# Kernel optimization log

Measured on AMD Instinct MI355X. Metric: run time of the kernel, lower is better.

## Reference

```python
import jax, jax.numpy as jnp
import numpy as np

B, S, T = 32, 512, 512
SRC_SIZE, TGT_SIZE, OUT_SIZE, NUM_HEAD = 2048, 1024, 1024, 8
HEAD_DIM = OUT_SIZE // NUM_HEAD  # 128


def setup_inputs() -> dict:
    key = jax.random.key(0)
    ks = jax.random.split(key, 12)
    src = jax.random.normal(ks[0], (B, S, SRC_SIZE), dtype=jnp.float32)
    tgt = jax.random.normal(ks[1], (B, T, TGT_SIZE), dtype=jnp.float32)
    # binary float masks (1=valid, 0=pad); guarantee at least one valid src per row
    src_mask = (jax.random.uniform(ks[2], (B, S)) > 0.3).astype(jnp.float32)
    src_mask = src_mask.at[:, 0].set(1.0)
    tgt_mask = (jax.random.uniform(ks[3], (B, T)) > 0.3).astype(jnp.float32)
    tgt_mask = tgt_mask.at[:, 0].set(1.0)
    # FCNet in this repo is weight_norm(Linear) with no activation at drop=0 -> plain Linear
    def lin(k, out_f, in_f):
        return jax.random.normal(k, (out_f, in_f), dtype=jnp.float32) / np.sqrt(in_f)
    W_src = lin(ks[4], 2 * OUT_SIZE, SRC_SIZE)
    b_src = jnp.zeros((2 * OUT_SIZE,), jnp.float32)
    W_tgt = lin(ks[5], OUT_SIZE, TGT_SIZE)
    b_tgt = jnp.zeros((OUT_SIZE,), jnp.float32)
    W_out = lin(ks[6], OUT_SIZE, OUT_SIZE + TGT_SIZE)
    b_out = jnp.zeros((OUT_SIZE,), jnp.float32)
    return {"src": src, "tgt": tgt, "src_mask": src_mask, "tgt_mask": tgt_mask,
            "W_src": W_src, "b_src": b_src, "W_tgt": W_tgt, "b_tgt": b_tgt,
            "W_out": W_out, "b_out": b_out}


def reference(src, tgt, src_mask, tgt_mask, W_src, b_src, W_tgt, b_tgt, W_out, b_out):
    b, s, _ = src.shape
    t = tgt.shape[1]
    # projections (FCNet == Linear here)
    src_trans = jnp.einsum('bsf,of->bso', src, W_src) + b_src        # [B,S,2D]
    tgt_trans = jnp.einsum('btf,of->bto', tgt, W_tgt) + b_tgt        # [B,T,D]
    src_trans = src_trans * src_mask[:, :, None]
    tgt_trans = tgt_trans * tgt_mask[:, :, None]
    src_key, src_val = jnp.split(src_trans, 2, axis=2)               # each [B,S,D]
    # contiguous per-head chunks == reshape
    k = src_key.reshape(b, s, NUM_HEAD, HEAD_DIM)
    v = src_val.reshape(b, s, NUM_HEAD, HEAD_DIM)
    q = tgt_trans.reshape(b, t, NUM_HEAD, HEAD_DIM)
    scores = jnp.einsum('bthd,bshd->bhts', q, k) / np.sqrt(HEAD_DIM)  # [B,H,T,S]
    scores = jnp.where(src_mask[:, None, None, :] == 0, -jnp.inf, scores)
    attn = jax.nn.softmax(scores, axis=-1)
    tgt_update = jnp.einsum('bhts,bshd->bthd', attn, v).reshape(b, t, OUT_SIZE)
    cat_tgt = jnp.concatenate([tgt, tgt_update], axis=2)             # [B,T,TGT+D]
    return jnp.einsum('btf,of->bto', cat_tgt, W_out) + b_out         # [B,T,D]
```

## Files before the change

kernel.cpp:

```cpp
#include <hip/hip_runtime.h>

typedef __attribute__((ext_vector_type(4))) float f32x4;
typedef __attribute__((ext_vector_type(8))) short short8;
typedef unsigned short u16;

__device__ __forceinline__ u16 f2bf(float f) {
  unsigned int u = __float_as_uint(f);
  return (u16)((u + 0x7fffu + ((u >> 16) & 1u)) >> 16);
}

__device__ __forceinline__ void gload16(const void* g, void* l) {
  __builtin_amdgcn_global_load_lds((const __attribute__((address_space(1))) void*)g,
                                   (__attribute__((address_space(3))) void*)l, 16, 0, 0);
}

__global__ void cvt_f32_bf16(const float* __restrict__ in, u16* __restrict__ out, int n4) {
  int i = blockIdx.x * blockDim.x + threadIdx.x;
  int stride = gridDim.x * blockDim.x;
  for (; i < n4; i += stride) {
    float4 v = ((const float4*)in)[i];
    ushort4 o;
    o.x = f2bf(v.x); o.y = f2bf(v.y); o.z = f2bf(v.z); o.w = f2bf(v.w);
    ((ushort4*)out)[i] = o;
  }
}

__global__ void cvt_tgt_strided(const float* __restrict__ in, u16* __restrict__ cat, int n4) {
  int i = blockIdx.x * blockDim.x + threadIdx.x;
  int stride = gridDim.x * blockDim.x;
  for (; i < n4; i += stride) {
    int e = i * 4;
    int row = e >> 10;
    int c = e & 1023;
    float4 v = ((const float4*)in)[i];
    ushort4 o;
    o.x = f2bf(v.x); o.y = f2bf(v.y); o.z = f2bf(v.z); o.w = f2bf(v.w);
    *(ushort4*)(cat + (size_t)row * 2048 + c) = o;
  }
}

template <bool MASK, bool OUTBF, bool VSPLIT>
__global__ __launch_bounds__(512) void gemm256(const u16* __restrict__ A, int lda,
                                               const u16* __restrict__ W,
                                               const float* __restrict__ bias,
                                               const float* __restrict__ rowmask,
                                               void* __restrict__ Cout, int ldc,
                                               int nbn, int K,
                                               u16* __restrict__ vTout) {
  __shared__ __align__(16) u16 lds[2 * 32768];
  const int tid = threadIdx.x;
  const int lane = tid & 63;
  const int wid = tid >> 6;
  const int lr = lane & 15, lh = lane >> 4;
  const int wm = wid >> 2;
  const int wn = wid & 3;

  const int nwg = gridDim.x;
  const int cpx = nwg >> 3;
  const int bid = (blockIdx.x & 7) * cpx + (blockIdx.x >> 3);
  const int bm = bid / nbn;
  const int bn = bid - bm * nbn;

  const int srow = tid >> 3;
  const int scol = ((tid & 7) ^ (srow & 7)) << 3;
  const u16* As0 = A + (size_t)(bm * 256 + srow) * lda + scol;
  const u16* Ws0 = W + (size_t)(bn * 256 + srow) * K + scol;

  auto stageA = [&](int h, int t, int buf) {
    char* d = (char*)lds + buf * 65536 + h * 16384 + tid * 16;
    const u16* s = As0 + (size_t)(h * 128) * lda + t * 64;
    gload16(s, d);
    gload16(s + (size_t)64 * lda, d + 8192);
  };
  auto stageB = [&](int h, int t, int buf) {
    char* d = (char*)lds + buf * 65536 + 32768 + h * 16384 + tid * 16;
    const u16* s = Ws0 + (size_t)(h * 128) * K + t * 64;
    gload16(s, d);
    gload16(s + (size_t)64 * K, d + 8192);
  };

  const int key = (lr & 7) << 4;
  const int sb0 = ((0 + lh) << 4) ^ key;
  const int sb1 = ((4 + lh) << 4) ^ key;
  const int arow = (wm * 64 + lr) * 128;
  const int brow = 32768 + (wn * 32 + lr) * 128;

  f32x4 acc[8][4];
#pragma unroll
  for (int m = 0; m < 8; ++m)
#pragma unroll
    for (int n = 0; n < 4; ++n) acc[m][n] = (f32x4){0.f, 0.f, 0.f, 0.f};

  const int NT = K >> 6;

  stageA(0, 0, 0); stageB(0, 0, 0); stageB(1, 0, 0); stageA(1, 0, 0);
  asm volatile("s_waitcnt vmcnt(4)" ::: "memory");
  __builtin_amdgcn_s_barrier();
  __builtin_amdgcn_sched_barrier(0);

  for (int t = 0; t < NT; ++t) {
    const int cur = t & 1, nxt = cur ^ 1;
    const char* Lb = (const char*)lds + cur * 65536;
    const bool pf = (t + 1 < NT);

    short8 a[4][2], b0[2][2], b1[2][2];

#pragma unroll
    for (int m = 0; m < 4; ++m) {
      a[m][0] = *(const short8*)(Lb + arow + m * 2048 + sb0);
      a[m][1] = *(const short8*)(Lb + arow + m * 2048 + sb1);
    }
#pragma unroll
    for (int n = 0; n < 2; ++n) {
      b0[n][0] = *(const short8*)(Lb + brow + n * 2048 + sb0);
      b0[n][1] = *(const short8*)(Lb + brow + n * 2048 + sb1);
    }
    if (pf) stageA(0, t + 1, nxt);
    asm volatile("s_waitcnt lgkmcnt(0)" ::: "memory");
    __builtin_amdgcn_sched_barrier(0);
    __builtin_amdgcn_s_setprio(1);
#pragma unroll
    for (int m = 0; m < 4; ++m)
#pragma unroll
      for (int n = 0; n < 2; ++n) {
        acc[m][n] = __builtin_amdgcn_mfma_f32_16x16x32_bf16(a[m][0], b0[n][0], acc[m][n], 0, 0, 0);
        acc[m][n] = __builtin_amdgcn_mfma_f32_16x16x32_bf16(a[m][1], b0[n][1], acc[m][n], 0, 0, 0);
      }
    __builtin_amdgcn_s_setprio(0);
    if (pf) { asm volatile("s_waitcnt vmcnt(4)" ::: "memory"); }
    else    { asm volatile("s_waitcnt vmcnt(2)" ::: "memory"); }
    __builtin_amdgcn_s_barrier();
    __builtin_amdgcn_sched_barrier(0);

#pragma unroll
    for (int n = 0; n < 2; ++n) {
      b1[n][0] = *(const short8*)(Lb + brow + 16384 + n * 2048 + sb0);
      b1[n][1] = *(const short8*)(Lb + brow + 16384 + n * 2048 + sb1);
    }
    if (pf) stageB(0, t + 1, nxt);
    asm volatile("s_waitcnt lgkmcnt(0)" ::: "memory");
    __builtin_amdgcn_sched_barrier(0);
    __builtin_amdgcn_s_setprio(1);
#pragma unroll
    for (int m = 0; m < 4; ++m)
#pragma unroll
      for (int n = 0; n < 2; ++n) {
        acc[m][2 + n] = __builtin_amdgcn_mfma_f32_16x16x32_bf16(a[m][0], b1[n][0], acc[m][2 + n], 0, 0, 0);
        acc[m][2 + n] = __builtin_amdgcn_mfma_f32_16x16x32_bf16(a[m][1], b1[n][1], acc[m][2 + n], 0, 0, 0);
      }
    __builtin_amdgcn_s_setprio(0);
    if (pf) { asm volatile("s_waitcnt vmcnt(4)" ::: "memory"); }
    else    { asm volatile("s_waitcnt vmcnt(0)" ::: "memory"); }
    __builtin_amdgcn_s_barrier();
    __builtin_amdgcn_sched_barrier(0);

#pragma unroll
    for (int m = 0; m < 4; ++m) {
      a[m][0] = *(const short8*)(Lb + 16384 + arow + m * 2048 + sb0);
      a[m][1] = *(const short8*)(Lb + 16384 + arow + m * 2048 + sb1);
    }
    if (pf) stageB(1, t + 1, nxt);
    asm volatile("s_waitcnt lgkmcnt(0)" ::: "memory");
    __builtin_amdgcn_sched_barrier(0);
    __builtin_amdgcn_s_setprio(1);
#pragma unroll
    for (int m = 0; m < 4; ++m)
#pragma unroll
      for (int n = 0; n < 2; ++n) {
        acc[4 + m][n] = __builtin_amdgcn_mfma_f32_16x16x32_bf16(a[m][0], b0[n][0], acc[4 + m][n], 0, 0, 0);
        acc[4 + m][n] = __builtin_amdgcn_mfma_f32_16x16x32_bf16(a[m][1], b0[n][1], acc[4 + m][n], 0, 0, 0);
      }
    __builtin_amdgcn_s_setprio(0);
    if (pf) { asm volatile("s_waitcnt vmcnt(4)" ::: "memory"); }
    __builtin_amdgcn_s_barrier();
    __builtin_amdgcn_sched_barrier(0);

    if (pf) stageA(1, t + 1, nxt);
    __builtin_amdgcn_s_setprio(1);
#pragma unroll
    for (int m = 0; m < 4; ++m)
#pragma unroll
      for (int n = 0; n < 2; ++n) {
        acc[4 + m][2 + n] = __builtin_amdgcn_mfma_f32_16x16x32_bf16(a[m][0], b1[n][0], acc[4 + m][2 + n], 0, 0, 0);
        acc[4 + m][2 + n] = __builtin_amdgcn_mfma_f32_16x16x32_bf16(a[m][1], b1[n][1], acc[4 + m][2 + n], 0, 0, 0);
      }
    __builtin_amdgcn_s_setprio(0);
    if (pf) { asm volatile("s_waitcnt vmcnt(4)" ::: "memory"); }
    __builtin_amdgcn_s_barrier();
    __builtin_amdgcn_sched_barrier(0);
  }

  const int r0 = bm * 256 + wm * 64 + lh * 4;
  const int c0 = bn * 256 + wn * 32 + lr;

  if constexpr (VSPLIT) {
    if (bn * 256 >= 1024) {
#pragma unroll
      for (int mi = 0; mi < 8; ++mi) {
        const int row_base = r0 + (mi >> 2) * 128 + (mi & 3) * 16;
        const int b = row_base >> 9;
        const int s = row_base & 511;
        float mk[4];
#pragma unroll
        for (int i = 0; i < 4; ++i) mk[i] = rowmask[row_base + i];
#pragma unroll
        for (int ni = 0; ni < 4; ++ni) {
          const int col = c0 + (ni >> 1) * 128 + (ni & 1) * 16;
          const float bv = bias[col];
          const int vcol = col - 1024;
          u16* vp = vTout + ((size_t)(b * 8 + (vcol >> 7)) * 128 + (vcol & 127)) * 512 + s;
          ushort4 o;
          o.x = f2bf((acc[mi][ni][0] + bv) * mk[0]);
          o.y = f2bf((acc[mi][ni][1] + bv) * mk[1]);
          o.z = f2bf((acc[mi][ni][2] + bv) * mk[2]);
          o.w = f2bf((acc[mi][ni][3] + bv) * mk[3]);
          *(ushort4*)vp = o;
        }
      }
      return;
    }
  }

#pragma unroll
  for (int mi = 0; mi < 8; ++mi) {
    const int row_base = r0 + (mi >> 2) * 128 + (mi & 3) * 16;
#pragma unroll
    for (int i = 0; i < 4; ++i) {
      const int row = row_base + i;
      float msk = 1.f;
      if constexpr (MASK) msk = rowmask[row];
#pragma unroll
      for (int ni = 0; ni < 4; ++ni) {
        const int col = c0 + (ni >> 1) * 128 + (ni & 1) * 16;
        float v = (acc[mi][ni][i] + bias[col]) * msk;
        if constexpr (OUTBF)
          ((u16*)Cout)[(size_t)row * ldc + col] = f2bf(v);
        else
          ((float*)Cout)[(size_t)row * ldc + col] = v;
      }
    }
  }
}

__global__ __launch_bounds__(256) void attn_fwd(const u16* __restrict__ q,
                                                const u16* __restrict__ kbuf,
                                                const u16* __restrict__ vT,
                                                const float* __restrict__ smask,
                                                u16* __restrict__ cat) {
  __shared__ __align__(16) u16 lds[20480];
  u16* Ks = lds;
  u16* Vt = lds + 8192;
  u16* Ps = lds + 16384;
  const int tid = threadIdx.x;
  const int lane = tid & 63;
  const int w = tid >> 6;
  const int lr = lane & 15, lh = lane >> 4;
  const int bh = blockIdx.x & 255;
  const int qb = blockIdx.x >> 8;
  const int b = bh >> 3;
  const int h = bh & 7;
  const int t0 = qb * 64 + w * 16;
  const float SCALE = 0.08838834764831845f;

  const u16* kbase = kbuf + (size_t)(b * 512) * 1024 + h * 128;
  const u16* vbase = vT + (size_t)bh * 128 * 512;

  short8 qf[4];
  {
    const u16* qp = q + (size_t)(b * 512 + t0 + lr) * 1024 + h * 128 + lh * 8;
#pragma unroll
    for (int kc = 0; kc < 4; ++kc) qf[kc] = *(const short8*)(qp + kc * 32);
  }

  f32x4 o[8];
#pragma unroll
  for (int dt = 0; dt < 8; ++dt) o[dt] = (f32x4){0.f, 0.f, 0.f, 0.f};
  float m_run[4], l_run[4];
#pragma unroll
  for (int i = 0; i < 4; ++i) { m_run[i] = -1e30f; l_run[i] = 0.f; }

  for (int s0 = 0; s0 < 512; s0 += 64) {
    __syncthreads();
#pragma unroll
    for (int it = 0; it < 4; ++it) {
      int idx = it * 256 + tid;
      int kr = idx >> 4, ks = idx & 15;
      gload16(kbase + (size_t)(s0 + kr) * 1024 + ((ks ^ (kr & 7)) * 8), (char*)Ks + idx * 16);
      int vr = idx >> 3, vs = idx & 7;
      gload16(vbase + (size_t)vr * 512 + s0 + ((vs ^ (vr & 7)) * 8), (char*)Vt + idx * 16);
    }
    asm volatile("s_waitcnt vmcnt(0)" ::: "memory");
    __syncthreads();

    f32x4 sc[4];
#pragma unroll
    for (int st = 0; st < 4; ++st) {
      f32x4 c = (f32x4){0.f, 0.f, 0.f, 0.f};
      const int row = st * 16 + lr;
#pragma unroll
      for (int kc = 0; kc < 4; ++kc) {
        short8 kb = *(const short8*)((const char*)Ks + row * 256 +
                                     ((kc * 64 + lh * 16) ^ ((row & 7) << 4)));
        c = __builtin_amdgcn_mfma_f32_16x16x32_bf16(qf[kc], kb, c, 0, 0, 0);
      }
      sc[st] = c;
    }

    float cm[4];
#pragma unroll
    for (int st = 0; st < 4; ++st) cm[st] = smask[b * 512 + s0 + st * 16 + lr];

    float pv[4][4], mx[4];
#pragma unroll
    for (int i = 0; i < 4; ++i) mx[i] = -1e30f;
#pragma unroll
    for (int st = 0; st < 4; ++st)
#pragma unroll
      for (int i = 0; i < 4; ++i) {
        float v = (cm[st] != 0.f) ? sc[st][i] * SCALE : -1e30f;
        pv[st][i] = v;
        mx[i] = fmaxf(mx[i], v);
      }
#pragma unroll
    for (int off = 1; off < 16; off <<= 1)
#pragma unroll
      for (int i = 0; i < 4; ++i) mx[i] = fmaxf(mx[i], __shfl_xor(mx[i], off));

    float m_new[4], scl[4], rs[4];
#pragma unroll
    for (int i = 0; i < 4; ++i) {
      m_new[i] = fmaxf(m_run[i], mx[i]);
      scl[i] = __expf(m_run[i] - m_new[i]);
      rs[i] = 0.f;
    }
#pragma unroll
    for (int st = 0; st < 4; ++st)
#pragma unroll
      for (int i = 0; i < 4; ++i) {
        float p = (cm[st] != 0.f) ? __expf(pv[st][i] - m_new[i]) : 0.f;
        pv[st][i] = p;
        rs[i] += p;
      }
#pragma unroll
    for (int off = 1; off < 16; off <<= 1)
#pragma unroll
      for (int i = 0; i < 4; ++i) rs[i] += __shfl_xor(rs[i], off);
#pragma unroll
    for (int i = 0; i < 4; ++i) {
      l_run[i] = l_run[i] * scl[i] + rs[i];
      m_run[i] = m_new[i];
    }
#pragma unroll
    for (int dt = 0; dt < 8; ++dt)
#pragma unroll
      for (int i = 0; i < 4; ++i) o[dt][i] *= scl[i];

#pragma unroll
    for (int st = 0; st < 4; ++st)
#pragma unroll
      for (int i = 0; i < 4; ++i) {
        const int prow = lh * 4 + i;
        Ps[w * 1024 + prow * 64 + (((st * 2 + (lr >> 3)) ^ (prow & 7)) * 8) + (lr & 7)] =
            f2bf(pv[st][i]);
      }

    short8 pa[2];
#pragma unroll
    for (int s2 = 0; s2 < 2; ++s2)
      pa[s2] = *(const short8*)(Ps + w * 1024 + lr * 64 + (((s2 * 4 + lh) ^ (lr & 7)) * 8));
#pragma unroll
    for (int dt = 0; dt < 8; ++dt) {
#pragma unroll
      for (int s2 = 0; s2 < 2; ++s2) {
        const int row = dt * 16 + lr;
        short8 vb = *(const short8*)((const char*)Vt + row * 128 +
                                     ((s2 * 64 + lh * 16) ^ ((row & 7) << 4)));
        o[dt] = __builtin_amdgcn_mfma_f32_16x16x32_bf16(pa[s2], vb, o[dt], 0, 0, 0);
      }
    }
  }

  float inv[4];
#pragma unroll
  for (int i = 0; i < 4; ++i) inv[i] = 1.f / l_run[i];
  u16* outp = cat + (size_t)(b * 512 + t0 + lh * 4) * 2048 + 1024 + h * 128 + lr;
#pragma unroll
  for (int dt = 0; dt < 8; ++dt)
#pragma unroll
    for (int i = 0; i < 4; ++i)
      outp[(size_t)i * 2048 + dt * 16] = f2bf(o[dt][i] * inv[i]);
}

extern "C" void kernel_launch(void* const* d_in, const int* in_sizes, int n_in,
                              void* d_out, int out_size, void* d_ws, size_t ws_size,
                              hipStream_t stream) {
  (void)in_sizes; (void)n_in; (void)out_size; (void)ws_size;
  const float* src      = (const float*)d_in[0];
  const float* tgt      = (const float*)d_in[1];
  const float* src_mask = (const float*)d_in[2];
  const float* tgt_mask = (const float*)d_in[3];
  const float* W_src    = (const float*)d_in[4];
  const float* b_src    = (const float*)d_in[5];
  const float* W_tgt    = (const float*)d_in[6];
  const float* b_tgt    = (const float*)d_in[7];
  const float* W_out    = (const float*)d_in[8];
  const float* b_out    = (const float*)d_in[9];

  char* ws = (char*)d_ws;
  u16* catb = (u16*)(ws);
  u16* kbuf = (u16*)(ws + 67108864);
  u16* vTb  = (u16*)(ws + 100663296);
  u16* qbuf = (u16*)(ws + 134217728);
  u16* wsrc = (u16*)(ws + 167772160);
  u16* wtgt = (u16*)(ws + 176160768);
  u16* wout = (u16*)(ws + 178257920);

  cvt_f32_bf16<<<2048, 256, 0, stream>>>(src, catb, 16384 * 2048 / 4);
  cvt_f32_bf16<<<1024, 256, 0, stream>>>(W_src, wsrc, 2048 * 2048 / 4);
  cvt_f32_bf16<<<256, 256, 0, stream>>>(W_tgt, wtgt, 1024 * 1024 / 4);
  cvt_f32_bf16<<<512, 256, 0, stream>>>(W_out, wout, 1024 * 2048 / 4);

  gemm256<true, true, true><<<512, 512, 0, stream>>>(catb, 2048, wsrc, b_src, src_mask,
                                                     kbuf, 1024, 8, 2048, vTb);

  cvt_tgt_strided<<<1024, 256, 0, stream>>>(tgt, catb, 16384 * 1024 / 4);

  gemm256<true, true, false><<<256, 512, 0, stream>>>(catb, 2048, wtgt, b_tgt, tgt_mask,
                                                      qbuf, 1024, 4, 1024, nullptr);

  attn_fwd<<<2048, 256, 0, stream>>>(qbuf, kbuf, vTb, src_mask, catb);

  gemm256<false, false, false><<<256, 512, 0, stream>>>(catb, 2048, wout, b_out, nullptr,
                                                        (float*)d_out, 1024, 4, 2048, nullptr);
}
```

Baseline: 392.6 us.

## Prefetch next tile's LDS fragments into registers across the GEMM main loop

Restructures the bf16 MFMA GEMM main loop so the first A/B fragments of the next K-tile are read from LDS during the last MFMA phase of the current tile, and uses partial lgkmcnt waits so LDS reads overlap MFMA work. The global-to-LDS staging order and vmcnt waits are rearranged to fit. This cuts the exposed LDS latency at the start of each iteration at the cost of extra registers (a2 buffer). The fragile hand-tuned waitcnt values risk races or lower occupancy.

```diff
diff --git a/kernel.cpp b/kernel.cpp
--- a/kernel.cpp
+++ b/kernel.cpp
@@ -94,29 +94,38 @@
   const int NT = K >> 6;
 
   stageA(0, 0, 0); stageB(0, 0, 0); stageB(1, 0, 0); stageA(1, 0, 0);
-  asm volatile("s_waitcnt vmcnt(4)" ::: "memory");
+  asm volatile("s_waitcnt vmcnt(2)" ::: "memory");
   __builtin_amdgcn_s_barrier();
   __builtin_amdgcn_sched_barrier(0);
+
+  short8 a[4][2], a2[4][2], b0[2][2], b1[2][2];
+  {
+    const char* Lb = (const char*)lds;
+#pragma unroll
+    for (int m = 0; m < 4; ++m) {
+      a[m][0] = *(const short8*)(Lb + arow + m * 2048 + sb0);
+      a[m][1] = *(const short8*)(Lb + arow + m * 2048 + sb1);
+    }
+#pragma unroll
+    for (int n = 0; n < 2; ++n) {
+      b0[n][0] = *(const short8*)(Lb + brow + n * 2048 + sb0);
+      b0[n][1] = *(const short8*)(Lb + brow + n * 2048 + sb1);
+    }
+  }
 
   for (int t = 0; t < NT; ++t) {
     const int cur = t & 1, nxt = cur ^ 1;
     const char* Lb = (const char*)lds + cur * 65536;
+    const char* Ln = (const char*)lds + nxt * 65536;
     const bool pf = (t + 1 < NT);
 
-    short8 a[4][2], b0[2][2], b1[2][2];
-
-#pragma unroll
-    for (int m = 0; m < 4; ++m) {
-      a[m][0] = *(const short8*)(Lb + arow + m * 2048 + sb0);
-      a[m][1] = *(const short8*)(Lb + arow + m * 2048 + sb1);
-    }
 #pragma unroll
     for (int n = 0; n < 2; ++n) {
-      b0[n][0] = *(const short8*)(Lb + brow + n * 2048 + sb0);
-      b0[n][1] = *(const short8*)(Lb + brow + n * 2048 + sb1);
-    }
-    if (pf) stageA(0, t + 1, nxt);
-    asm volatile("s_waitcnt lgkmcnt(0)" ::: "memory");
+      b1[n][0] = *(const short8*)(Lb + brow + 16384 + n * 2048 + sb0);
+      b1[n][1] = *(const short8*)(Lb + brow + 16384 + n * 2048 + sb1);
+    }
+    if (pf) { stageA(0, t + 1, nxt); stageB(0, t + 1, nxt); }
+    asm volatile("s_waitcnt lgkmcnt(4)" ::: "memory");
     __builtin_amdgcn_sched_barrier(0);
     __builtin_amdgcn_s_setprio(1);
 #pragma unroll
@@ -125,28 +134,6 @@
       for (int n = 0; n < 2; ++n) {
         acc[m][n] = __builtin_amdgcn_mfma_f32_16x16x32_bf16(a[m][0], b0[n][0], acc[m][n], 0, 0, 0);
         acc[m][n] = __builtin_amdgcn_mfma_f32_16x16x32_bf16(a[m][1], b0[n][1], acc[m][n], 0, 0, 0);
-      }
-    __builtin_amdgcn_s_setprio(0);
-    if (pf) { asm volatile("s_waitcnt vmcnt(4)" ::: "memory"); }
-    else    { asm volatile("s_waitcnt vmcnt(2)" ::: "memory"); }
-    __builtin_amdgcn_s_barrier();
-    __builtin_amdgcn_sched_barrier(0);
-
-#pragma unroll
-    for (int n = 0; n < 2; ++n) {
-      b1[n][0] = *(const short8*)(Lb + brow + 16384 + n * 2048 + sb0);
-      b1[n][1] = *(const short8*)(Lb + brow + 16384 + n * 2048 + sb1);
-    }
-    if (pf) stageB(0, t + 1, nxt);
-    asm volatile("s_waitcnt lgkmcnt(0)" ::: "memory");
-    __builtin_amdgcn_sched_barrier(0);
-    __builtin_amdgcn_s_setprio(1);
-#pragma unroll
-    for (int m = 0; m < 4; ++m)
-#pragma unroll
-      for (int n = 0; n < 2; ++n) {
-        acc[m][2 + n] = __builtin_amdgcn_mfma_f32_16x16x32_bf16(a[m][0], b1[n][0], acc[m][2 + n], 0, 0, 0);
-        acc[m][2 + n] = __builtin_amdgcn_mfma_f32_16x16x32_bf16(a[m][1], b1[n][1], acc[m][2 + n], 0, 0, 0);
       }
     __builtin_amdgcn_s_setprio(0);
     if (pf) { asm volatile("s_waitcnt vmcnt(4)" ::: "memory"); }
@@ -156,10 +143,25 @@
 
 #pragma unroll
     for (int m = 0; m < 4; ++m) {
-      a[m][0] = *(const short8*)(Lb + 16384 + arow + m * 2048 + sb0);
-      a[m][1] = *(const short8*)(Lb + 16384 + arow + m * 2048 + sb1);
+      a2[m][0] = *(const short8*)(Lb + 16384 + arow + m * 2048 + sb0);
+      a2[m][1] = *(const short8*)(Lb + 16384 + arow + m * 2048 + sb1);
     }
     if (pf) stageB(1, t + 1, nxt);
+    asm volatile("s_waitcnt lgkmcnt(8)" ::: "memory");
+    __builtin_amdgcn_sched_barrier(0);
+    __builtin_amdgcn_s_setprio(1);
+#pragma unroll
+    for (int m = 0; m < 4; ++m)
+#pragma unroll
+      for (int n = 0; n < 2; ++n) {
+        acc[m][2 + n] = __builtin_amdgcn_mfma_f32_16x16x32_bf16(a[m][0], b1[n][0], acc[m][2 + n], 0, 0, 0);
+        acc[m][2 + n] = __builtin_amdgcn_mfma_f32_16x16x32_bf16(a[m][1], b1[n][1], acc[m][2 + n], 0, 0, 0);
+      }
+    __builtin_amdgcn_s_setprio(0);
+    __builtin_amdgcn_s_barrier();
+    __builtin_amdgcn_sched_barrier(0);
+
+    if (pf) stageA(1, t + 1, nxt);
     asm volatile("s_waitcnt lgkmcnt(0)" ::: "memory");
     __builtin_amdgcn_sched_barrier(0);
     __builtin_amdgcn_s_setprio(1);
@@ -167,25 +169,38 @@
     for (int m = 0; m < 4; ++m)
 #pragma unroll
       for (int n = 0; n < 2; ++n) {
-        acc[4 + m][n] = __builtin_amdgcn_mfma_f32_16x16x32_bf16(a[m][0], b0[n][0], acc[4 + m][n], 0, 0, 0);
-        acc[4 + m][n] = __builtin_amdgcn_mfma_f32_16x16x32_bf16(a[m][1], b0[n][1], acc[4 + m][n], 0, 0, 0);
+        acc[4 + m][n] = __builtin_amdgcn_mfma_f32_16x16x32_bf16(a2[m][0], b0[n][0], acc[4 + m][n], 0, 0, 0);
+        acc[4 + m][n] = __builtin_amdgcn_mfma_f32_16x16x32_bf16(a2[m][1], b0[n][1], acc[4 + m][n], 0, 0, 0);
       }
     __builtin_amdgcn_s_setprio(0);
     if (pf) { asm volatile("s_waitcnt vmcnt(4)" ::: "memory"); }
+    else    { asm volatile("s_waitcnt vmcnt(0)" ::: "memory"); }
     __builtin_amdgcn_s_barrier();
     __builtin_amdgcn_sched_barrier(0);
 
-    if (pf) stageA(1, t + 1, nxt);
+    if (pf) {
+#pragma unroll
+      for (int m = 0; m < 4; ++m) {
+        a[m][0] = *(const short8*)(Ln + arow + m * 2048 + sb0);
+        a[m][1] = *(const short8*)(Ln + arow + m * 2048 + sb1);
+      }
+#pragma unroll
+      for (int n = 0; n < 2; ++n) {
+        b0[n][0] = *(const short8*)(Ln + brow + n * 2048 + sb0);
+        b0[n][1] = *(const short8*)(Ln + brow + n * 2048 + sb1);
+      }
+    }
+    __builtin_amdgcn_sched_barrier(0);
     __builtin_amdgcn_s_setprio(1);
 #pragma unroll
     for (int m = 0; m < 4; ++m)
 #pragma unroll
       for (int n = 0; n < 2; ++n) {
-        acc[4 + m][2 + n] = __builtin_amdgcn_mfma_f32_16x16x32_bf16(a[m][0], b1[n][0], acc[4 + m][2 + n], 0, 0, 0);
-        acc[4 + m][2 + n] = __builtin_amdgcn_mfma_f32_16x16x32_bf16(a[m][1], b1[n][1], acc[4 + m][2 + n], 0, 0, 0);
+        acc[4 + m][2 + n] = __builtin_amdgcn_mfma_f32_16x16x32_bf16(a2[m][0], b1[n][0], acc[4 + m][2 + n], 0, 0, 0);
+        acc[4 + m][2 + n] = __builtin_amdgcn_mfma_f32_16x16x32_bf16(a2[m][1], b1[n][1], acc[4 + m][2 + n], 0, 0, 0);
       }
     __builtin_amdgcn_s_setprio(0);
-    if (pf) { asm volatile("s_waitcnt vmcnt(4)" ::: "memory"); }
+    if (pf) { asm volatile("s_waitcnt vmcnt(2)" ::: "memory"); }
     __builtin_amdgcn_s_barrier();
     __builtin_amdgcn_sched_barrier(0);
   }
```

After: 391.5 us. About the same (-0.3%).
